# Performance work log

Hardware: AMD Instinct MI355X
Metric: run time of the kernel (lower is better)

## Reference

```python
import jax, jax.numpy as jnp
import numpy as np

K_GAUSS = 10
HIDDEN = 512


def setup_inputs() -> dict:
    key = jax.random.key(0)
    k1, k2, k3 = jax.random.split(key, 3)
    lstm_out = jax.random.normal(k1, (16, 1024, HIDDEN), dtype=jnp.float32)
    char_seq = jax.random.uniform(k2, (16, 600, 80), dtype=jnp.float32)
    # Dense(3*k_gaussians): small init so exp(params) stays in a sane range
    W = jax.random.normal(k3, (HIDDEN, 3 * K_GAUSS), dtype=jnp.float32) * 0.02
    bias = jnp.zeros((3 * K_GAUSS,), dtype=jnp.float32)
    return {"lstm_out": lstm_out, "char_seq": char_seq, "W": W, "bias": bias}


def reference(lstm_out, char_seq, W, bias):
    # lstm_out: [B,T,H], char_seq: [B,U,A]
    U = char_seq.shape[1]
    params = jnp.einsum('bth,hp->btp', lstm_out, W) + bias  # [B,T,3K]
    exp_params = jnp.exp(params)
    a, b, k = jnp.split(exp_params, 3, axis=2)              # each [B,T,K]
    u = jnp.arange(U, dtype=lstm_out.dtype).reshape(1, 1, U, 1)  # char indices
    # gaussian mixture window weights phi[b,t,u] = sum_k a*exp(-b*(k-u)^2)
    gaussians = a[:, :, None, :] * jnp.exp(-b[:, :, None, :] * jnp.square(k[:, :, None, :] - u))  # [B,T,U,K]
    char_weights = jnp.sum(gaussians, axis=3)               # [B,T,U]
    # alphabet_window[b,t,a] = sum_u phi[b,t,u] * char_seq[b,u,a]
    return jnp.einsum('btu,bua->bta', char_weights, char_seq)
```

## Files before the change

### kernel.cpp

```cpp
#include <hip/hip_runtime.h>
#include <math.h>

#define BB 16
#define TD 1024
#define HD 512
#define UD 600
#define AD 80
#define KG 10
#define PC 30
#define PP 32

#define LOG2E 1.4426950408889634f

#if __has_builtin(__builtin_amdgcn_exp2f)
#define EXP2F(x) __builtin_amdgcn_exp2f(x)
#else
#define EXP2F(x) exp2f(x)
#endif

#define KP_ROWS 64

__global__ __launch_bounds__(1024) void k_params(const float* __restrict__ x,
                                                 const float* __restrict__ W,
                                                 const float* __restrict__ bias,
                                                 float* __restrict__ ep) {
    __shared__ float red[8 * KP_ROWS * 31];

    int tid = threadIdx.x;
    int wv = __builtin_amdgcn_readfirstlane(tid >> 6);
    int lane = tid & 63;
    long row = (long)blockIdx.x * KP_ROWS + lane;

    const float* xr = x + row * HD + wv * 32;
    const float* wr = W + (long)wv * 32 * PC;

    float4 xv[8];
    #pragma unroll
    for (int i = 0; i < 8; i++) xv[i] = *(const float4*)(xr + i * 4);

    float acc[PC];
    #pragma unroll
    for (int c = 0; c < PC; c++) acc[c] = 0.f;

    #pragma unroll
    for (int i = 0; i < 8; i++) {
        #pragma unroll
        for (int j = 0; j < 4; j++) {
            float xs = (j == 0) ? xv[i].x : (j == 1) ? xv[i].y
                     : (j == 2) ? xv[i].z : xv[i].w;
            #pragma unroll
            for (int c = 0; c < PC; c++)
                acc[c] += xs * wr[(i * 4 + j) * PC + c];
        }
    }

    if (wv >= 8) {
        #pragma unroll
        for (int c = 0; c < PC; c++)
            red[(wv - 8) * (KP_ROWS * 31) + lane * 31 + c] = acc[c];
    }
    __syncthreads();
    if (wv < 8) {
        #pragma unroll
        for (int c = 0; c < PC; c++)
            red[wv * (KP_ROWS * 31) + lane * 31 + c] += acc[c];
    }
    __syncthreads();

    for (int idx = tid; idx < KP_ROWS * PC; idx += 1024) {
        int r = idx / PC, c = idx - r * PC;
        float v = 0.f;
        #pragma unroll
        for (int s = 0; s < 8; s++)
            v += red[s * (KP_ROWS * 31) + r * 31 + c];
        float e = __expf(v + bias[c]);
        float val = (c >= 10 && c < 20) ? (-e * LOG2E) : e;
        ep[((long)blockIdx.x * KP_ROWS + r) * PP + c] = val;
    }
}

#define TT 32
#define UC 40
#define NCHUNK 15
#define NTHR 320

__global__ __launch_bounds__(NTHR) void k_main(const float* __restrict__ ep,
                                               const float* __restrict__ cs,
                                               float* __restrict__ out) {
    __shared__ float params_l[TT * 36];
    __shared__ float cs_l[UC * AD];
    __shared__ float phi2[TT * 44];
    __shared__ float range_l[2];

    int tid = threadIdx.x;
    int b = blockIdx.y;
    int t0 = blockIdx.x * TT;
    long r0 = (long)b * TD + t0;

    if (tid < 256) {
        float4 v = *(const float4*)(ep + r0 * PP + tid * 4);
        int tt_ = tid >> 3, j = (tid & 7) * 4;
        *(float4*)&params_l[tt_ * 36 + j] = v;
    }
    __syncthreads();

    int tt = tid & 31;
    int sub = tid >> 5;
    float pa[KG], pnb[KG], pk[KG];
    #pragma unroll
    for (int q = 0; q < KG; q++) {
        pa[q]  = params_l[tt * 36 + q];
        pnb[q] = params_l[tt * 36 + 10 + q];
        pk[q]  = params_l[tt * 36 + 20 + q];
    }

    {
        float lo = 1e30f, hi = -1e30f;
        #pragma unroll
        for (int q = 0; q < KG; q++) {
            float bits = 46.f + fmaxf(0.f, __log2f(pa[q]));
            float w = __fsqrt_rn(bits / (-pnb[q]));
            lo = fminf(lo, pk[q] - w);
            hi = fmaxf(hi, pk[q] + w);
        }
        if (tid < 64) {
            #pragma unroll
            for (int m = 1; m < 64; m <<= 1) {
                lo = fminf(lo, __shfl_xor(lo, m));
                hi = fmaxf(hi, __shfl_xor(hi, m));
            }
            if (tid == 0) { range_l[0] = lo; range_l[1] = hi; }
        }
    }
    __syncthreads();
    float lo_m = fminf(fmaxf(range_l[0], 0.f), (float)(UD - 1));
    float hi_m = fminf(fmaxf(range_l[1], 0.f), (float)(UD - 1));
    int ch_lo = (int)lo_m / UC;
    int ch_hi = (int)hi_m / UC;
    if (ch_lo > ch_hi) ch_lo = ch_hi;

    int tx = tid % 20;
    int ty = tid / 20;
    float4 acc0 = {0.f, 0.f, 0.f, 0.f};
    float4 acc1 = {0.f, 0.f, 0.f, 0.f};

    const float* csb = cs + (long)b * UD * AD;

    for (int ch = ch_lo; ch <= ch_hi; ch++) {
        int u0 = ch * UC;
        __syncthreads();

        for (int idx = tid; idx < (UC * AD) / 4; idx += NTHR) {
            *(float4*)&cs_l[idx * 4] = *(const float4*)&csb[u0 * AD + idx * 4];
        }

        float ph[4];
        #pragma unroll
        for (int i = 0; i < 4; i++) {
            float uf = (float)(u0 + sub * 4 + i);
            float ss = 0.f;
            #pragma unroll
            for (int q = 0; q < KG; q++) {
                float d = uf - pk[q];
                ss += pa[q] * EXP2F(pnb[q] * d * d);
            }
            ph[i] = ss;
        }
        *(float4*)&phi2[tt * 44 + sub * 4] = make_float4(ph[0], ph[1], ph[2], ph[3]);
        __syncthreads();

        #pragma unroll 2
        for (int g = 0; g < 10; g++) {
            float4 p0 = *(const float4*)&phi2[(ty * 2) * 44 + g * 4];
            float4 p1 = *(const float4*)&phi2[(ty * 2 + 1) * 44 + g * 4];
            #pragma unroll
            for (int i = 0; i < 4; i++) {
                float4 c4 = *(const float4*)&cs_l[(g * 4 + i) * AD + tx * 4];
                float pi0 = (i == 0) ? p0.x : (i == 1) ? p0.y : (i == 2) ? p0.z : p0.w;
                float pi1 = (i == 0) ? p1.x : (i == 1) ? p1.y : (i == 2) ? p1.z : p1.w;
                acc0.x += pi0 * c4.x; acc0.y += pi0 * c4.y;
                acc0.z += pi0 * c4.z; acc0.w += pi0 * c4.w;
                acc1.x += pi1 * c4.x; acc1.y += pi1 * c4.y;
                acc1.z += pi1 * c4.z; acc1.w += pi1 * c4.w;
            }
        }
    }

    long t = r0 + ty * 2;
    *(float4*)(out + t * AD + tx * 4) = acc0;
    *(float4*)(out + (t + 1) * AD + tx * 4) = acc1;
}

extern "C" void kernel_launch(void* const* d_in, const int* in_sizes, int n_in,
                              void* d_out, int out_size, void* d_ws, size_t ws_size,
                              hipStream_t stream) {
    const float* lstm = (const float*)d_in[0];
    const float* cs   = (const float*)d_in[1];
    const float* W    = (const float*)d_in[2];
    const float* bias = (const float*)d_in[3];
    float* out = (float*)d_out;

    float* ep = (float*)d_ws;

    k_params<<<(BB * TD) / KP_ROWS, 1024, 0, stream>>>(lstm, W, bias, ep);
    dim3 grid(TD / TT, BB);
    k_main<<<grid, NTHR, 0, stream>>>(ep, cs, out);
}
```

Measured before the change: 98.27 us.

## Compute projection GEMM with split-bf16 MFMA instead of scalar FP32 FMAs

Replaces the scalar FP32 projection kernel with one that uses MFMA 16x16x32 bf16 instructions. Both the activations and the weights are split into hi and lo bf16 parts, and three MFMAs per tile recover near-FP32 accuracy. A small prep kernel repacks W into the MFMA fragment layout on every call. The projection kernel now uses 256-thread blocks over 16 rows. This adds an extra launch and conversion ALU work, and accuracy falls slightly below full FP32.

```diff
diff --git a/kernel.cpp b/kernel.cpp
--- a/kernel.cpp
+++ b/kernel.cpp
@@ -18,64 +18,90 @@
 #define EXP2F(x) exp2f(x)
 #endif
 
-#define KP_ROWS 64
-
-__global__ __launch_bounds__(1024) void k_params(const float* __restrict__ x,
-                                                 const float* __restrict__ W,
-                                                 const float* __restrict__ bias,
-                                                 float* __restrict__ ep) {
-    __shared__ float red[8 * KP_ROWS * 31];
+typedef short v8s __attribute__((ext_vector_type(8)));
+typedef float v4f __attribute__((ext_vector_type(4)));
+
+__device__ inline unsigned short f2bf(float f) {
+    unsigned u = __float_as_uint(f);
+    return (unsigned short)((u + 0x7FFF + ((u >> 16) & 1)) >> 16);
+}
+
+__global__ void k_wprep(const float* __restrict__ W,
+                        unsigned short* __restrict__ Wfh,
+                        unsigned short* __restrict__ Wfl) {
+    int p = blockIdx.x * 256 + threadIdx.x;
+    for (; p < 32768; p += 256 * 32) {
+        int j = p & 7, l = (p >> 3) & 63, n = (p >> 9) & 1, kt = p >> 10;
+        int k = kt * 32 + ((l >> 4) * 8) + j;
+        int c = n * 16 + (l & 15);
+        float v = (c < PC) ? W[k * PC + c] : 0.f;
+        unsigned short h = f2bf(v);
+        float hi_f = __uint_as_float(((unsigned)h) << 16);
+        Wfh[p] = h;
+        Wfl[p] = f2bf(v - hi_f);
+    }
+}
+
+__global__ __launch_bounds__(256) void k_params(const float* __restrict__ x,
+                                                const unsigned short* __restrict__ Wfh,
+                                                const unsigned short* __restrict__ Wfl,
+                                                const float* __restrict__ bias,
+                                                float* __restrict__ ep) {
+    __shared__ float red[4 * 16 * 33];
 
     int tid = threadIdx.x;
-    int wv = __builtin_amdgcn_readfirstlane(tid >> 6);
-    int lane = tid & 63;
-    long row = (long)blockIdx.x * KP_ROWS + lane;
-
-    const float* xr = x + row * HD + wv * 32;
-    const float* wr = W + (long)wv * 32 * PC;
-
-    float4 xv[8];
+    int wv = tid >> 6;
+    int l = tid & 63;
+    int quad = l >> 4, m = l & 15;
+    long row0 = (long)blockIdx.x * 16;
+
+    const float* xr = x + (row0 + m) * HD + wv * 128 + quad * 8;
+
+    v4f acc[2] = {{0.f, 0.f, 0.f, 0.f}, {0.f, 0.f, 0.f, 0.f}};
+
     #pragma unroll
-    for (int i = 0; i < 8; i++) xv[i] = *(const float4*)(xr + i * 4);
-
-    float acc[PC];
+    for (int kt = 0; kt < 4; kt++) {
+        float4 xa = *(const float4*)(xr + kt * 32);
+        float4 xb = *(const float4*)(xr + kt * 32 + 4);
+        float xf[8] = {xa.x, xa.y, xa.z, xa.w, xb.x, xb.y, xb.z, xb.w};
+        v8s ah, al;
+        #pragma unroll
+        for (int j = 0; j < 8; j++) {
+            unsigned short h = f2bf(xf[j]);
+            ah[j] = (short)h;
+            al[j] = (short)f2bf(xf[j] - __uint_as_float(((unsigned)h) << 16));
+        }
+        int ktg = wv * 4 + kt;
+        #pragma unroll
+        for (int n = 0; n < 2; n++) {
+            uint4 uh = *(const uint4*)&Wfh[((ktg * 2 + n) * 64 + l) * 8];
+            uint4 ul = *(const uint4*)&Wfl[((ktg * 2 + n) * 64 + l) * 8];
+            v8s bh, bl;
+            __builtin_memcpy(&bh, &uh, 16);
+            __builtin_memcpy(&bl, &ul, 16);
+            acc[n] = __builtin_amdgcn_mfma_f32_16x16x32_bf16(ah, bh, acc[n], 0, 0, 0);
+            acc[n] = __builtin_amdgcn_mfma_f32_16x16x32_bf16(al, bh, acc[n], 0, 0, 0);
+            acc[n] = __builtin_amdgcn_mfma_f32_16x16x32_bf16(ah, bl, acc[n], 0, 0, 0);
+        }
+    }
+
     #pragma unroll
-    for (int c = 0; c < PC; c++) acc[c] = 0.f;
-
-    #pragma unroll
-    for (int i = 0; i < 8; i++) {
-        #pragma unroll
-        for (int j = 0; j < 4; j++) {
-            float xs = (j == 0) ? xv[i].x : (j == 1) ? xv[i].y
-                     : (j == 2) ? xv[i].z : xv[i].w;
-            #pragma unroll
-            for (int c = 0; c < PC; c++)
-                acc[c] += xs * wr[(i * 4 + j) * PC + c];
-        }
-    }
-
-    if (wv >= 8) {
-        #pragma unroll
-        for (int c = 0; c < PC; c++)
-            red[(wv - 8) * (KP_ROWS * 31) + lane * 31 + c] = acc[c];
-    }
+    for (int n = 0; n < 2; n++)
+        #pragma unroll
+        for (int r = 0; r < 4; r++)
+            red[wv * 528 + (quad * 4 + r) * 33 + n * 16 + m] = acc[n][r];
     __syncthreads();
-    if (wv < 8) {
-        #pragma unroll
-        for (int c = 0; c < PC; c++)
-            red[wv * (KP_ROWS * 31) + lane * 31 + c] += acc[c];
-    }
-    __syncthreads();
-
-    for (int idx = tid; idx < KP_ROWS * PC; idx += 1024) {
-        int r = idx / PC, c = idx - r * PC;
-        float v = 0.f;
-        #pragma unroll
-        for (int s = 0; s < 8; s++)
-            v += red[s * (KP_ROWS * 31) + r * 31 + c];
-        float e = __expf(v + bias[c]);
-        float val = (c >= 10 && c < 20) ? (-e * LOG2E) : e;
-        ep[((long)blockIdx.x * KP_ROWS + r) * PP + c] = val;
+
+    for (int idx = tid; idx < 16 * PP; idx += 256) {
+        int mm = idx >> 5, c = idx & 31;
+        float val = 0.f;
+        if (c < PC) {
+            float s = red[0 * 528 + mm * 33 + c] + red[1 * 528 + mm * 33 + c]
+                    + red[2 * 528 + mm * 33 + c] + red[3 * 528 + mm * 33 + c];
+            float e = __expf(s + bias[c]);
+            val = (c >= 10 && c < 20) ? (-e * LOG2E) : e;
+        }
+        ep[(row0 + mm) * PP + c] = val;
     }
 }
 
@@ -125,9 +151,9 @@
         }
         if (tid < 64) {
             #pragma unroll
-            for (int m = 1; m < 64; m <<= 1) {
-                lo = fminf(lo, __shfl_xor(lo, m));
-                hi = fmaxf(hi, __shfl_xor(hi, m));
+            for (int mk = 1; mk < 64; mk <<= 1) {
+                lo = fminf(lo, __shfl_xor(lo, mk));
+                hi = fmaxf(hi, __shfl_xor(hi, mk));
             }
             if (tid == 0) { range_l[0] = lo; range_l[1] = hi; }
         }
@@ -201,8 +227,11 @@
     float* out = (float*)d_out;
 
     float* ep = (float*)d_ws;
-
-    k_params<<<(BB * TD) / KP_ROWS, 1024, 0, stream>>>(lstm, W, bias, ep);
+    unsigned short* Wfh = (unsigned short*)((char*)d_ws + (16384L * PP * 4));
+    unsigned short* Wfl = Wfh + 32768;
+
+    k_wprep<<<32, 256, 0, stream>>>(W, Wfh, Wfl);
+    k_params<<<(BB * TD) / 16, 256, 0, stream>>>(lstm, Wfh, Wfl, bias, ep);
     dim3 grid(TD / TT, BB);
     k_main<<<grid, NTHR, 0, stream>>>(ep, cs, out);
 }
```

Result: faster. 93.00 us (-5.4%).
